# Performance work log

Measured on AMD Instinct MI355X. Metric: run time of the kernel, lower is better.

The kernel has to match this reference:

```python
import jax, jax.numpy as jnp
import numpy as np

N, F_IN, E = 50000, 128, 800000
HID, HEADS, EMB = 32, 8, 64
NEG_SLOPE = 0.2


def gat_conv(x, src, dst, W_src, W_dst, att_src, att_dst, bias, heads, out_ch, concat):
    n = x.shape[0]
    h_src = (x @ W_src).reshape(n, heads, out_ch)   # [N,H,C]
    h_dst = (x @ W_dst).reshape(n, heads, out_ch)
    a_src = jnp.sum(h_src * att_src, axis=-1)       # [N,H]
    a_dst = jnp.sum(h_dst * att_dst, axis=-1)
    e = jax.nn.leaky_relu(a_src[src] + a_dst[dst], NEG_SLOPE)  # [E,H]
    # segment softmax over destination nodes (stable, max detached as in PyG)
    m = jax.ops.segment_max(e, dst, num_segments=n)
    m = jnp.where(jnp.isfinite(m), m, 0.0)
    ex = jnp.exp(e - jax.lax.stop_gradient(m)[dst])
    denom = jax.ops.segment_sum(ex, dst, num_segments=n)
    alpha = ex / (denom[dst] + 1e-16)               # [E,H]
    msg = h_src[src] * alpha[:, :, None]            # [E,H,C]
    out = jax.ops.segment_sum(msg, dst, num_segments=n)  # [N,H,C]
    if concat:
        out = out.reshape(n, heads * out_ch)
    else:
        out = out.mean(axis=1)
    return out + bias


def setup_inputs() -> dict:
    key = jax.random.key(0)
    ks = jax.random.split(key, 12)
    g = lambda k, shape: jax.random.normal(k, shape, dtype=jnp.float32) * (1.0 / np.sqrt(shape[0]))
    x = jax.random.normal(ks[0], (N, F_IN), dtype=jnp.float32)
    edge_index = jax.random.randint(ks[1], (2, E), 0, N, dtype=jnp.int64)
    return {
        "x": x,
        "edge_index": edge_index,
        "W_src1": g(ks[2], (F_IN, HEADS * HID)),
        "W_dst1": g(ks[3], (F_IN, HEADS * HID)),
        "att_src1": g(ks[4], (HEADS, HID)) * 0.1,
        "att_dst1": g(ks[5], (HEADS, HID)) * 0.1,
        "b1": jnp.zeros((HEADS * HID,), dtype=jnp.float32),
        "W_src2": g(ks[6], (HEADS * HID, EMB)),
        "W_dst2": g(ks[7], (HEADS * HID, EMB)),
        "att_src2": g(ks[8], (1, EMB)) * 0.1,
        "att_dst2": g(ks[9], (1, EMB)) * 0.1,
        "b2": jnp.zeros((EMB,), dtype=jnp.float32),
    }


def reference(x, edge_index, W_src1, W_dst1, att_src1, att_dst1, b1,
              W_src2, W_dst2, att_src2, att_dst2, b2):
    src, dst = edge_index[0], edge_index[1]
    h = gat_conv(x, src, dst, W_src1, W_dst1, att_src1, att_dst1, b1, HEADS, HID, True)
    h = jax.nn.relu(h)
    out = gat_conv(h, src, dst, W_src2, W_dst2, att_src2, att_dst2, b2, 1, EMB, False)
    return out
```

## Files before the change

### kernel.cpp

```cpp
#include <hip/hip_runtime.h>
#include <hip/hip_bf16.h>
#include <cstdint>
#include <cstddef>

#define NN    50000
#define FIN   128
#define EE    800000
#define HID_  32
#define HEADS_ 8
#define EMB_  64
#define NEG   0.2f
#define CAP   64
#define NB_PREP 202
#define NB_HIST 782
#define NB_XCNV 3125
#define LOG2E 1.4426950408889634f

typedef short bf16x8 __attribute__((ext_vector_type(8)));
typedef float f32x4  __attribute__((ext_vector_type(4)));
typedef float f32x2  __attribute__((ext_vector_type(2)));

static __device__ __forceinline__ ushort f2bf(float f){
    uint u = __float_as_uint(f);
    uint r = (u + 0x7FFFu + ((u >> 16) & 1u)) >> 16;
    return (ushort)r;
}
static __device__ __forceinline__ float bf2f(ushort u){
    return __uint_as_float(((uint)u) << 16);
}
static __device__ __forceinline__ f32x2 bfpair(uint u){
    f32x2 r;
    r[0] = __uint_as_float(u << 16);
    r[1] = __uint_as_float(u & 0xffff0000u);
    return r;
}
static __device__ __forceinline__ float pexp(float t){
    return __builtin_amdgcn_exp2f(fmaxf(t, NEG * t));
}

__global__ __launch_bounds__(256) void k_prep_hist(const float* __restrict__ Wsrc1, const float* __restrict__ Wdst1,
                                                   const float* __restrict__ asrc1, const float* __restrict__ adst1,
                                                   const float* __restrict__ Wsrc2, const float* __restrict__ Wdst2,
                                                   const float* __restrict__ asrc2, const float* __restrict__ adst2,
                                                   ushort* __restrict__ wt1bf, float* __restrict__ wt2,
                                                   ushort* __restrict__ w1t, ushort* __restrict__ w2t,
                                                   const int* __restrict__ src, const int* __restrict__ dst,
                                                   int* __restrict__ deg, int* __restrict__ col,
                                                   const float* __restrict__ x, ushort* __restrict__ xbf){
    if (blockIdx.x >= NB_PREP + NB_HIST){
        int t = (blockIdx.x - NB_PREP - NB_HIST) * 256 + threadIdx.x;
        const float4* xp = (const float4*)(x + (size_t)t * 8);
        float4 f0 = xp[0], f1 = xp[1];
        ushort4 u0, u1;
        u0.x = f2bf(f0.x); u0.y = f2bf(f0.y); u0.z = f2bf(f0.z); u0.w = f2bf(f0.w);
        u1.x = f2bf(f1.x); u1.y = f2bf(f1.y); u1.z = f2bf(f1.z); u1.w = f2bf(f1.w);
        ushort4* op = (ushort4*)(xbf + (size_t)t * 8);
        op[0] = u0; op[1] = u1;
        return;
    }
    if (blockIdx.x >= NB_PREP){
        int t = (blockIdx.x - NB_PREP) * 256 + threadIdx.x;
        int e0 = t * 4;
        if (e0 + 3 < EE){
            int4 d4 = *(const int4*)&dst[e0];
            int4 s4 = *(const int4*)&src[e0];
            int r0 = atomicAdd(&deg[d4.x], 1);
            int r1 = atomicAdd(&deg[d4.y], 1);
            int r2 = atomicAdd(&deg[d4.z], 1);
            int r3 = atomicAdd(&deg[d4.w], 1);
            col[d4.x * CAP + r0] = s4.x;
            col[d4.y * CAP + r1] = s4.y;
            col[d4.z * CAP + r2] = s4.z;
            col[d4.w * CAP + r3] = s4.w;
        } else {
            for (int e = e0; e < EE; ++e){
                int d = dst[e];
                int r = atomicAdd(&deg[d], 1);
                col[d * CAP + r] = src[e];
            }
        }
        return;
    }
    int idx = blockIdx.x * blockDim.x + threadIdx.x;
    if (idx < 2048){
        int f = idx >> 4, j = idx & 15;
        const float* W; const float* a; int h;
        if (j < 8) { W = Wsrc1; a = asrc1; h = j; } else { W = Wdst1; a = adst1; h = j - 8; }
        float s = 0.f;
        #pragma unroll
        for (int c = 0; c < HID_; ++c)
            s += W[(size_t)f * (HEADS_ * HID_) + h * HID_ + c] * a[h * HID_ + c];
        wt1bf[j * 128 + f] = f2bf(s * LOG2E);
    } else if (idx < 2560){
        int t = idx - 2048;
        int f = t >> 1, j = t & 1;
        const float* W = j ? Wdst2 : Wsrc2;
        const float* a = j ? adst2 : asrc2;
        float s = 0.f;
        #pragma unroll
        for (int c = 0; c < EMB_; ++c) s += W[(size_t)f * EMB_ + c] * a[c];
        wt2[j * 256 + f] = s * LOG2E;
    } else if (idx < 35328){
        int t = idx - 2560;
        int n = t >> 7, k = t & 127;
        w1t[t] = f2bf(Wsrc1[(size_t)k * 256 + n]);
    } else if (idx < 51712){
        int t = idx - 35328;
        int n = t >> 8, k = t & 255;
        w2t[t] = f2bf(Wsrc2[(size_t)k * 64 + n]);
    }
}

__global__ __launch_bounds__(256) void k_gemm1_mfma(const ushort* __restrict__ xbf,
                                                    const ushort* __restrict__ w1t,
                                                    const ushort* __restrict__ wt1bf,
                                                    ushort* __restrict__ c,
                                                    float* __restrict__ a_src1,
                                                    float* __restrict__ a_dst1){
    __shared__ ushort As[64][136];
    __shared__ ushort Bs[128][136];
    __shared__ ushort Bsa[16][136];
    const int tid = threadIdx.x;
    const int m0 = blockIdx.x * 64;
    const int n0 = blockIdx.y * 128;
    #pragma unroll
    for (int i = 0; i < 4; ++i){
        int idx = tid + i * 256;
        int r = idx >> 4, c8 = idx & 15;
        int m = m0 + r;
        ushort4 v0 = make_ushort4(0,0,0,0), v1 = make_ushort4(0,0,0,0);
        if (m < NN){
            const ushort4* s4 = (const ushort4*)&xbf[(size_t)m * FIN + c8 * 8];
            v0 = s4[0]; v1 = s4[1];
        }
        *(ushort4*)&As[r][c8 * 8]     = v0;
        *(ushort4*)&As[r][c8 * 8 + 4] = v1;
    }
    #pragma unroll
    for (int i = 0; i < 8; ++i){
        int idx = tid + i * 256;
        int r = idx >> 4, c8 = idx & 15;
        const ushort4* s4 = (const ushort4*)&w1t[(size_t)(n0 + r) * 128 + c8 * 8];
        *(ushort4*)&Bs[r][c8 * 8]     = s4[0];
        *(ushort4*)&Bs[r][c8 * 8 + 4] = s4[1];
    }
    if (blockIdx.y == 0){
        int r = tid >> 4, c8 = tid & 15;
        const ushort4* s4 = (const ushort4*)&wt1bf[r * 128 + c8 * 8];
        *(ushort4*)&Bsa[r][c8 * 8]     = s4[0];
        *(ushort4*)&Bsa[r][c8 * 8 + 4] = s4[1];
    }
    __syncthreads();
    const int lane = tid & 63;
    const int w    = tid >> 6;
    const int mr   = lane & 15;
    const int kg   = lane >> 4;
    f32x4 acc[8];
    #pragma unroll
    for (int i = 0; i < 8; ++i) acc[i] = (f32x4){0.f, 0.f, 0.f, 0.f};
    f32x4 acca = (f32x4){0.f, 0.f, 0.f, 0.f};
    #pragma unroll
    for (int ks = 0; ks < 4; ++ks){
        bf16x8 a = *(const bf16x8*)&As[w * 16 + mr][ks * 32 + kg * 8];
        #pragma unroll
        for (int nf = 0; nf < 8; ++nf){
            bf16x8 b = *(const bf16x8*)&Bs[nf * 16 + mr][ks * 32 + kg * 8];
            acc[nf] = __builtin_amdgcn_mfma_f32_16x16x32_bf16(a, b, acc[nf], 0, 0, 0);
        }
        if (blockIdx.y == 0){
            bf16x8 ba = *(const bf16x8*)&Bsa[mr][ks * 32 + kg * 8];
            acca = __builtin_amdgcn_mfma_f32_16x16x32_bf16(a, ba, acca, 0, 0, 0);
        }
    }
    #pragma unroll
    for (int nf = 0; nf < 8; ++nf){
        int colb = n0 + nf * 16 + mr;
        #pragma unroll
        for (int r = 0; r < 4; ++r){
            int row = m0 + w * 16 + kg * 4 + r;
            if (row < NN) c[(size_t)row * 256 + colb] = f2bf(acc[nf][r]);
        }
    }
    if (blockIdx.y == 0){
        int j = mr;
        #pragma unroll
        for (int r = 0; r < 4; ++r){
            int row = m0 + w * 16 + kg * 4 + r;
            if (row < NN){
                if (j < 8) a_src1[(size_t)row * 8 + j]       = acca[r];
                else       a_dst1[(size_t)row * 8 + (j - 8)] = acca[r];
            }
        }
    }
}

__global__ __launch_bounds__(256) void k_agg1(const ushort* __restrict__ hsrc, const float* __restrict__ a_src,
                                              const float* __restrict__ a_dst, const int* __restrict__ deg,
                                              const int* __restrict__ col, const float* __restrict__ b1,
                                              const float* __restrict__ wt2,
                                              ushort* __restrict__ hout_bf,
                                              float* __restrict__ a_src2, float* __restrict__ a_dst2){
    int node = blockIdx.x * 4 + (threadIdx.x >> 6);
    if (node >= NN) return;
    int lane = threadIdx.x & 63;
    int head = lane >> 3;
    float ad = a_dst[(size_t)node * 8 + head];
    const uint2* h2 = (const uint2*)hsrc;
    f32x2 accA = (f32x2){0.f, 0.f};
    f32x2 accB = (f32x2){0.f, 0.f};
    float den = 0.f;
    int b = node * CAP, en = b + deg[node];
    int i = b;
    for (; i + 4 <= en; i += 4){
        int s0 = col[i], s1 = col[i+1], s2 = col[i+2], s3 = col[i+3];
        float e0 = a_src[(size_t)s0 * 8 + head];
        float e1 = a_src[(size_t)s1 * 8 + head];
        float e2 = a_src[(size_t)s2 * 8 + head];
        float e3 = a_src[(size_t)s3 * 8 + head];
        uint2 v0 = h2[(size_t)s0 * 64 + lane];
        uint2 v1 = h2[(size_t)s1 * 64 + lane];
        uint2 v2 = h2[(size_t)s2 * 64 + lane];
        uint2 v3 = h2[(size_t)s3 * 64 + lane];
        float p0 = pexp(e0 + ad);
        float p1 = pexp(e1 + ad);
        float p2 = pexp(e2 + ad);
        float p3 = pexp(e3 + ad);
        accA += p0 * bfpair(v0.x); accB += p0 * bfpair(v0.y);
        accA += p1 * bfpair(v1.x); accB += p1 * bfpair(v1.y);
        accA += p2 * bfpair(v2.x); accB += p2 * bfpair(v2.y);
        accA += p3 * bfpair(v3.x); accB += p3 * bfpair(v3.y);
        den += p0 + p1 + p2 + p3;
    }
    for (; i < en; ++i){
        int s = col[i];
        float p = pexp(a_src[(size_t)s * 8 + head] + ad);
        uint2 v = h2[(size_t)s * 64 + lane];
        accA += p * bfpair(v.x);
        accB += p * bfpair(v.y);
        den += p;
    }
    float inv = 1.f / (den + 1e-16f);
    float4 bb = ((const float4*)b1)[lane];
    float4 o;
    o.x = fmaxf(accA[0] * inv + bb.x, 0.f);
    o.y = fmaxf(accA[1] * inv + bb.y, 0.f);
    o.z = fmaxf(accB[0] * inv + bb.z, 0.f);
    o.w = fmaxf(accB[1] * inv + bb.w, 0.f);
    ushort4 ob; ob.x = f2bf(o.x); ob.y = f2bf(o.y); ob.z = f2bf(o.z); ob.w = f2bf(o.w);
    ((ushort4*)hout_bf)[(size_t)node * 64 + lane] = ob;
    float4 ws4 = ((const float4*)wt2)[lane];
    float4 wd4 = ((const float4*)(wt2 + 256))[lane];
    float ss2 = o.x*ws4.x + o.y*ws4.y + o.z*ws4.z + o.w*ws4.w;
    float sd2 = o.x*wd4.x + o.y*wd4.y + o.z*wd4.z + o.w*wd4.w;
    #pragma unroll
    for (int off = 32; off > 0; off >>= 1){
        ss2 += __shfl_xor(ss2, off);
        sd2 += __shfl_xor(sd2, off);
    }
    if (lane == 0){ a_src2[node] = ss2; a_dst2[node] = sd2; }
}

__global__ __launch_bounds__(256) void k_gemm2_mfma(const ushort* __restrict__ hbf,
                                                    const ushort* __restrict__ w2t,
                                                    ushort* __restrict__ c2){
    __shared__ ushort As[64][264];
    __shared__ ushort Bs[64][264];
    const int tid = threadIdx.x;
    const int m0 = blockIdx.x * 64;
    #pragma unroll
    for (int i = 0; i < 8; ++i){
        int idx = tid + i * 256;
        int r = idx >> 5, c8 = idx & 31;
        int m = m0 + r;
        ushort4 v0 = make_ushort4(0,0,0,0), v1 = make_ushort4(0,0,0,0);
        if (m < NN){
            const ushort4* s4 = (const ushort4*)&hbf[(size_t)m * 256 + c8 * 8];
            v0 = s4[0]; v1 = s4[1];
        }
        *(ushort4*)&As[r][c8 * 8]     = v0;
        *(ushort4*)&As[r][c8 * 8 + 4] = v1;
    }
    #pragma unroll
    for (int i = 0; i < 8; ++i){
        int idx = tid + i * 256;
        int r = idx >> 5, c8 = idx & 31;
        const ushort4* s4 = (const ushort4*)&w2t[(size_t)r * 256 + c8 * 8];
        *(ushort4*)&Bs[r][c8 * 8]     = s4[0];
        *(ushort4*)&Bs[r][c8 * 8 + 4] = s4[1];
    }
    __syncthreads();
    const int lane = tid & 63;
    const int w    = tid >> 6;
    const int mr   = lane & 15;
    const int kg   = lane >> 4;
    f32x4 acc[4];
    #pragma unroll
    for (int i = 0; i < 4; ++i) acc[i] = (f32x4){0.f, 0.f, 0.f, 0.f};
    #pragma unroll
    for (int ks = 0; ks < 8; ++ks){
        bf16x8 a = *(const bf16x8*)&As[w * 16 + mr][ks * 32 + kg * 8];
        #pragma unroll
        for (int nf = 0; nf < 4; ++nf){
            bf16x8 b = *(const bf16x8*)&Bs[nf * 16 + mr][ks * 32 + kg * 8];
            acc[nf] = __builtin_amdgcn_mfma_f32_16x16x32_bf16(a, b, acc[nf], 0, 0, 0);
        }
    }
    #pragma unroll
    for (int nf = 0; nf < 4; ++nf){
        int colb = nf * 16 + mr;
        #pragma unroll
        for (int r = 0; r < 4; ++r){
            int row = m0 + w * 16 + kg * 4 + r;
            if (row < NN) c2[(size_t)row * 64 + colb] = f2bf(acc[nf][r]);
        }
    }
}

__global__ __launch_bounds__(256) void k_agg2(const ushort* __restrict__ h2bf, const float* __restrict__ a_src2,
                                              const float* __restrict__ a_dst2, const int* __restrict__ deg,
                                              const int* __restrict__ col, const float* __restrict__ b2,
                                              float* __restrict__ out){
    int node = blockIdx.x * 4 + (threadIdx.x >> 6);
    if (node >= NN) return;
    int lane = threadIdx.x & 63;
    int pair = lane >> 5;
    int cl   = lane & 31;
    float ad = a_dst2[node];
    float acc0 = 0.f, acc1 = 0.f, den = 0.f;
    int b = node * CAP, en = b + deg[node];
    int i = b;
    for (; i + 8 <= en; i += 8){
        int i0 = i + pair, i1 = i + 2 + pair, i2 = i + 4 + pair, i3 = i + 6 + pair;
        int s0 = col[i0], s1 = col[i1], s2 = col[i2], s3 = col[i3];
        float e0 = a_src2[s0], e1 = a_src2[s1], e2 = a_src2[s2], e3 = a_src2[s3];
        uint u0 = *(const uint*)&h2bf[(size_t)s0 * 64 + cl * 2];
        uint u1 = *(const uint*)&h2bf[(size_t)s1 * 64 + cl * 2];
        uint u2 = *(const uint*)&h2bf[(size_t)s2 * 64 + cl * 2];
        uint u3 = *(const uint*)&h2bf[(size_t)s3 * 64 + cl * 2];
        float p0 = pexp(e0 + ad);
        float p1 = pexp(e1 + ad);
        float p2 = pexp(e2 + ad);
        float p3 = pexp(e3 + ad);
        acc0 += p0*bf2f((ushort)(u0 & 0xffff)) + p1*bf2f((ushort)(u1 & 0xffff))
              + p2*bf2f((ushort)(u2 & 0xffff)) + p3*bf2f((ushort)(u3 & 0xffff));
        acc1 += p0*bf2f((ushort)(u0 >> 16))    + p1*bf2f((ushort)(u1 >> 16))
              + p2*bf2f((ushort)(u2 >> 16))    + p3*bf2f((ushort)(u3 >> 16));
        den += p0 + p1 + p2 + p3;
    }
    for (; i < en; i += 2){
        int ie = i + pair;
        bool v = ie < en;
        int s = col[v ? ie : en - 1];
        float e = a_src2[s];
        uint u = *(const uint*)&h2bf[(size_t)s * 64 + cl * 2];
        float p = v ? pexp(e + ad) : 0.f;
        acc0 += p * bf2f((ushort)(u & 0xffff));
        acc1 += p * bf2f((ushort)(u >> 16));
        den  += p;
    }
    acc0 += __shfl_xor(acc0, 32);
    acc1 += __shfl_xor(acc1, 32);
    den  += __shfl_xor(den , 32);
    if (lane < 32){
        float inv = 1.f / (den + 1e-16f);
        float2 o;
        o.x = acc0 * inv + b2[cl * 2];
        o.y = acc1 * inv + b2[cl * 2 + 1];
        *(float2*)&out[(size_t)node * 64 + cl * 2] = o;
    }
}

extern "C" void kernel_launch(void* const* d_in, const int* in_sizes, int n_in,
                              void* d_out, int out_size, void* d_ws, size_t ws_size,
                              hipStream_t stream){
    const float* x        = (const float*)d_in[0];
    const int*   ei       = (const int*)  d_in[1];
    const float* Wsrc1    = (const float*)d_in[2];
    const float* Wdst1    = (const float*)d_in[3];
    const float* att_src1 = (const float*)d_in[4];
    const float* att_dst1 = (const float*)d_in[5];
    const float* b1       = (const float*)d_in[6];
    const float* Wsrc2    = (const float*)d_in[7];
    const float* Wdst2    = (const float*)d_in[8];
    const float* att_src2 = (const float*)d_in[9];
    const float* att_dst2 = (const float*)d_in[10];
    const float* b2       = (const float*)d_in[11];
    float* out = (float*)d_out;
    const int* srcp = ei;
    const int* dstp = ei + EE;

    char* base = (char*)d_ws;
    ushort* hbf1   = (ushort*)base;  base += (size_t)NN * 256 * 2;
    ushort* hrel   = (ushort*)base;  base += (size_t)NN * 256 * 2;
    ushort* h2bf   = (ushort*)base;  base += (size_t)NN * 64 * 2;
    ushort* xbf    = (ushort*)base;  base += (size_t)NN * FIN * 2;
    float*  a_src1 = (float*)base;   base += (size_t)NN * 8 * 4;
    float*  a_dst1 = (float*)base;   base += (size_t)NN * 8 * 4;
    float*  a_src2 = (float*)base;   base += (size_t)NN * 4;
    float*  a_dst2 = (float*)base;   base += (size_t)NN * 4;
    ushort* wt1bf  = (ushort*)base;  base += 2048 * 2;
    float*  wt2    = (float*)base;   base += 512 * 4;
    ushort* w1t    = (ushort*)base;  base += 32768 * 2;
    ushort* w2t    = (ushort*)base;  base += 16384 * 2;
    int* deg     = (int*)base;       base += (size_t)NN * 4;
    int* col     = (int*)base;       base += (size_t)NN * CAP * 4;

    (void)hipMemsetAsync(deg, 0, NN * sizeof(int), stream);

    k_prep_hist<<<NB_PREP + NB_HIST + NB_XCNV, 256, 0, stream>>>(
        Wsrc1, Wdst1, att_src1, att_dst1,
        Wsrc2, Wdst2, att_src2, att_dst2,
        wt1bf, wt2, w1t, w2t,
        srcp, dstp, deg, col, x, xbf);
    dim3 g1((NN + 63) / 64, 2);
    k_gemm1_mfma<<<g1, 256, 0, stream>>>(xbf, w1t, wt1bf, hbf1, a_src1, a_dst1);
    k_agg1<<<(NN + 3) / 4, 256, 0, stream>>>(hbf1, a_src1, a_dst1, deg, col, b1, wt2,
                                             hrel, a_src2, a_dst2);
    k_gemm2_mfma<<<(NN + 63) / 64, 256, 0, stream>>>(hrel, w2t, h2bf);
    k_agg2<<<(NN + 3) / 4, 256, 0, stream>>>(h2bf, a_src2, a_dst2, deg, col, b2, out);
}
```

Measured before the change: 195.9 us.

## Move edge histogram into GEMM1 launch, zero degrees in prep, read B from global

Drops the memset by zeroing deg inside the prep kernel, and moves the edge-bucketing histogram blocks out of prep into the same launch as the first MFMA GEMM, so atomics overlap with GEMM work. The GEMM no longer stages W1 and the attention-weight rows in LDS. It loads B fragments straight from global (L2-cached) into registers, which cuts LDS use and raises occupancy. The cost is redundant global reads of the weights per block, plus heterogeneous blocks in one grid. The deg zeroing must finish before the histogram atomics, which the kernel boundary guarantees.

```diff
diff --git a/kernel.cpp b/kernel.cpp
--- a/kernel.cpp
+++ b/kernel.cpp
@@ -14,6 +14,7 @@
 #define NB_PREP 202
 #define NB_HIST 782
 #define NB_XCNV 3125
+#define NB_G1   1564
 #define LOG2E 1.4426950408889634f
 
 typedef short bf16x8 __attribute__((ext_vector_type(8)));
@@ -38,17 +39,16 @@
     return __builtin_amdgcn_exp2f(fmaxf(t, NEG * t));
 }
 
-__global__ __launch_bounds__(256) void k_prep_hist(const float* __restrict__ Wsrc1, const float* __restrict__ Wdst1,
-                                                   const float* __restrict__ asrc1, const float* __restrict__ adst1,
-                                                   const float* __restrict__ Wsrc2, const float* __restrict__ Wdst2,
-                                                   const float* __restrict__ asrc2, const float* __restrict__ adst2,
-                                                   ushort* __restrict__ wt1bf, float* __restrict__ wt2,
-                                                   ushort* __restrict__ w1t, ushort* __restrict__ w2t,
-                                                   const int* __restrict__ src, const int* __restrict__ dst,
-                                                   int* __restrict__ deg, int* __restrict__ col,
-                                                   const float* __restrict__ x, ushort* __restrict__ xbf){
-    if (blockIdx.x >= NB_PREP + NB_HIST){
-        int t = (blockIdx.x - NB_PREP - NB_HIST) * 256 + threadIdx.x;
+__global__ __launch_bounds__(256) void k_prep(const float* __restrict__ Wsrc1, const float* __restrict__ Wdst1,
+                                              const float* __restrict__ asrc1, const float* __restrict__ adst1,
+                                              const float* __restrict__ Wsrc2, const float* __restrict__ Wdst2,
+                                              const float* __restrict__ asrc2, const float* __restrict__ adst2,
+                                              ushort* __restrict__ wt1bf, float* __restrict__ wt2,
+                                              ushort* __restrict__ w1t, ushort* __restrict__ w2t,
+                                              int* __restrict__ deg,
+                                              const float* __restrict__ x, ushort* __restrict__ xbf){
+    if (blockIdx.x >= NB_PREP){
+        int t = (blockIdx.x - NB_PREP) * 256 + threadIdx.x;
         const float4* xp = (const float4*)(x + (size_t)t * 8);
         float4 f0 = xp[0], f1 = xp[1];
         ushort4 u0, u1;
@@ -58,8 +58,48 @@
         op[0] = u0; op[1] = u1;
         return;
     }
-    if (blockIdx.x >= NB_PREP){
-        int t = (blockIdx.x - NB_PREP) * 256 + threadIdx.x;
+    int idx = blockIdx.x * blockDim.x + threadIdx.x;
+    if (idx < NN) deg[idx] = 0;
+    if (idx < 2048){
+        int f = idx >> 4, j = idx & 15;
+        const float* W; const float* a; int h;
+        if (j < 8) { W = Wsrc1; a = asrc1; h = j; } else { W = Wdst1; a = adst1; h = j - 8; }
+        float s = 0.f;
+        #pragma unroll
+        for (int c = 0; c < HID_; ++c)
+            s += W[(size_t)f * (HEADS_ * HID_) + h * HID_ + c] * a[h * HID_ + c];
+        wt1bf[j * 128 + f] = f2bf(s * LOG2E);
+    } else if (idx < 2560){
+        int t = idx - 2048;
+        int f = t >> 1, j = t & 1;
+        const float* W = j ? Wdst2 : Wsrc2;
+        const float* a = j ? adst2 : asrc2;
+        float s = 0.f;
+        #pragma unroll
+        for (int c = 0; c < EMB_; ++c) s += W[(size_t)f * EMB_ + c] * a[c];
+        wt2[j * 256 + f] = s * LOG2E;
+    } else if (idx < 35328){
+        int t = idx - 2560;
+        int n = t >> 7, k = t & 127;
+        w1t[t] = f2bf(Wsrc1[(size_t)k * 256 + n]);
+    } else if (idx < 51712){
+        int t = idx - 35328;
+        int n = t >> 8, k = t & 255;
+        w2t[t] = f2bf(Wsrc2[(size_t)k * 64 + n]);
+    }
+}
+
+__global__ __launch_bounds__(256) void k_hist_gemm1(const ushort* __restrict__ xbf,
+                                                    const ushort* __restrict__ w1t,
+                                                    const ushort* __restrict__ wt1bf,
+                                                    ushort* __restrict__ c,
+                                                    float* __restrict__ a_src1,
+                                                    float* __restrict__ a_dst1,
+                                                    const int* __restrict__ src, const int* __restrict__ dst,
+                                                    int* __restrict__ deg, int* __restrict__ col){
+    __shared__ ushort As[64][136];
+    if (blockIdx.x < NB_HIST){
+        int t = blockIdx.x * 256 + threadIdx.x;
         int e0 = t * 4;
         if (e0 + 3 < EE){
             int4 d4 = *(const int4*)&dst[e0];
@@ -81,48 +121,10 @@
         }
         return;
     }
-    int idx = blockIdx.x * blockDim.x + threadIdx.x;
-    if (idx < 2048){
-        int f = idx >> 4, j = idx & 15;
-        const float* W; const float* a; int h;
-        if (j < 8) { W = Wsrc1; a = asrc1; h = j; } else { W = Wdst1; a = adst1; h = j - 8; }
-        float s = 0.f;
-        #pragma unroll
-        for (int c = 0; c < HID_; ++c)
-            s += W[(size_t)f * (HEADS_ * HID_) + h * HID_ + c] * a[h * HID_ + c];
-        wt1bf[j * 128 + f] = f2bf(s * LOG2E);
-    } else if (idx < 2560){
-        int t = idx - 2048;
-        int f = t >> 1, j = t & 1;
-        const float* W = j ? Wdst2 : Wsrc2;
-        const float* a = j ? adst2 : asrc2;
-        float s = 0.f;
-        #pragma unroll
-        for (int c = 0; c < EMB_; ++c) s += W[(size_t)f * EMB_ + c] * a[c];
-        wt2[j * 256 + f] = s * LOG2E;
-    } else if (idx < 35328){
-        int t = idx - 2560;
-        int n = t >> 7, k = t & 127;
-        w1t[t] = f2bf(Wsrc1[(size_t)k * 256 + n]);
-    } else if (idx < 51712){
-        int t = idx - 35328;
-        int n = t >> 8, k = t & 255;
-        w2t[t] = f2bf(Wsrc2[(size_t)k * 64 + n]);
-    }
-}
-
-__global__ __launch_bounds__(256) void k_gemm1_mfma(const ushort* __restrict__ xbf,
-                                                    const ushort* __restrict__ w1t,
-                                                    const ushort* __restrict__ wt1bf,
-                                                    ushort* __restrict__ c,
-                                                    float* __restrict__ a_src1,
-                                                    float* __restrict__ a_dst1){
-    __shared__ ushort As[64][136];
-    __shared__ ushort Bs[128][136];
-    __shared__ ushort Bsa[16][136];
-    const int tid = threadIdx.x;
-    const int m0 = blockIdx.x * 64;
-    const int n0 = blockIdx.y * 128;
+    const int bid2 = blockIdx.x - NB_HIST;
+    const int tid  = threadIdx.x;
+    const int m0   = (bid2 >> 1) * 64;
+    const int n0   = (bid2 & 1) * 128;
     #pragma unroll
     for (int i = 0; i < 4; ++i){
         int idx = tid + i * 256;
@@ -136,20 +138,6 @@
         *(ushort4*)&As[r][c8 * 8]     = v0;
         *(ushort4*)&As[r][c8 * 8 + 4] = v1;
     }
-    #pragma unroll
-    for (int i = 0; i < 8; ++i){
-        int idx = tid + i * 256;
-        int r = idx >> 4, c8 = idx & 15;
-        const ushort4* s4 = (const ushort4*)&w1t[(size_t)(n0 + r) * 128 + c8 * 8];
-        *(ushort4*)&Bs[r][c8 * 8]     = s4[0];
-        *(ushort4*)&Bs[r][c8 * 8 + 4] = s4[1];
-    }
-    if (blockIdx.y == 0){
-        int r = tid >> 4, c8 = tid & 15;
-        const ushort4* s4 = (const ushort4*)&wt1bf[r * 128 + c8 * 8];
-        *(ushort4*)&Bsa[r][c8 * 8]     = s4[0];
-        *(ushort4*)&Bsa[r][c8 * 8 + 4] = s4[1];
-    }
     __syncthreads();
     const int lane = tid & 63;
     const int w    = tid >> 6;
@@ -159,18 +147,22 @@
     #pragma unroll
     for (int i = 0; i < 8; ++i) acc[i] = (f32x4){0.f, 0.f, 0.f, 0.f};
     f32x4 acca = (f32x4){0.f, 0.f, 0.f, 0.f};
+    const ushort* bbase  = w1t   + (size_t)(n0 + mr) * 128;
+    const ushort* babase = wt1bf + (size_t)mr * 128;
     #pragma unroll
     for (int ks = 0; ks < 4; ++ks){
         bf16x8 a = *(const bf16x8*)&As[w * 16 + mr][ks * 32 + kg * 8];
-        #pragma unroll
-        for (int nf = 0; nf < 8; ++nf){
-            bf16x8 b = *(const bf16x8*)&Bs[nf * 16 + mr][ks * 32 + kg * 8];
-            acc[nf] = __builtin_amdgcn_mfma_f32_16x16x32_bf16(a, b, acc[nf], 0, 0, 0);
-        }
-        if (blockIdx.y == 0){
-            bf16x8 ba = *(const bf16x8*)&Bsa[mr][ks * 32 + kg * 8];
+        bf16x8 b[8];
+        #pragma unroll
+        for (int nf = 0; nf < 8; ++nf)
+            b[nf] = *(const bf16x8*)&bbase[(size_t)nf * 16 * 128 + ks * 32 + kg * 8];
+        bf16x8 ba;
+        if (n0 == 0) ba = *(const bf16x8*)&babase[ks * 32 + kg * 8];
+        #pragma unroll
+        for (int nf = 0; nf < 8; ++nf)
+            acc[nf] = __builtin_amdgcn_mfma_f32_16x16x32_bf16(a, b[nf], acc[nf], 0, 0, 0);
+        if (n0 == 0)
             acca = __builtin_amdgcn_mfma_f32_16x16x32_bf16(a, ba, acca, 0, 0, 0);
-        }
     }
     #pragma unroll
     for (int nf = 0; nf < 8; ++nf){
@@ -181,7 +173,7 @@
             if (row < NN) c[(size_t)row * 256 + colb] = f2bf(acc[nf][r]);
         }
     }
-    if (blockIdx.y == 0){
+    if (n0 == 0){
         int j = mr;
         #pragma unroll
         for (int r = 0; r < 4; ++r){
@@ -405,15 +397,13 @@
     int* deg     = (int*)base;       base += (size_t)NN * 4;
     int* col     = (int*)base;       base += (size_t)NN * CAP * 4;
 
-    (void)hipMemsetAsync(deg, 0, NN * sizeof(int), stream);
-
-    k_prep_hist<<<NB_PREP + NB_HIST + NB_XCNV, 256, 0, stream>>>(
+    k_prep<<<NB_PREP + NB_XCNV, 256, 0, stream>>>(
         Wsrc1, Wdst1, att_src1, att_dst1,
         Wsrc2, Wdst2, att_src2, att_dst2,
-        wt1bf, wt2, w1t, w2t,
-        srcp, dstp, deg, col, x, xbf);
-    dim3 g1((NN + 63) / 64, 2);
-    k_gemm1_mfma<<<g1, 256, 0, stream>>>(xbf, w1t, wt1bf, hbf1, a_src1, a_dst1);
+        wt1bf, wt2, w1t, w2t, deg, x, xbf);
+    k_hist_gemm1<<<NB_HIST + NB_G1, 256, 0, stream>>>(
+        xbf, w1t, wt1bf, hbf1, a_src1, a_dst1,
+        srcp, dstp, deg, col);
     k_agg1<<<(NN + 3) / 4, 256, 0, stream>>>(hbf1, a_src1, a_dst1, deg, col, b1, wt2,
                                              hrel, a_src2, a_dst2);
     k_gemm2_mfma<<<(NN + 63) / 64, 256, 0, stream>>>(hrel, w2t, h2bf);
```

Result: no change. 196.0 us (+0.1%).
